# Performance work log

Hardware: AMD Instinct MI355X
Metric: run time of the kernel (lower is better)

Reference implementation:

```python
import jax, jax.numpy as jnp
import numpy as np

N = 50000
E = 800000
IN_DIM = 128
HEADS = 8
OUT_DIM = 32
NEG_SLOPE = 0.2


def setup_inputs() -> dict:
    key = jax.random.key(0)
    k1, k2, k3, k4, k5 = jax.random.split(key, 5)
    x = jax.random.normal(k1, (N, IN_DIM), dtype=jnp.float32)
    edge_index = jax.random.randint(k2, (2, E), 0, N, dtype=jnp.int64)
    batch = jnp.zeros((N,), dtype=jnp.int64)
    # GATConv params: glorot-style scale
    W = jax.random.normal(k3, (IN_DIM, HEADS * OUT_DIM), dtype=jnp.float32) * (1.0 / np.sqrt(IN_DIM))
    att_src = jax.random.normal(k4, (HEADS, OUT_DIM), dtype=jnp.float32) * (1.0 / np.sqrt(OUT_DIM))
    att_dst = jax.random.normal(k5, (HEADS, OUT_DIM), dtype=jnp.float32) * (1.0 / np.sqrt(OUT_DIM))
    bias = jnp.zeros((OUT_DIM,), dtype=jnp.float32)
    return {"x": x, "edge_index": edge_index, "batch": batch,
            "W": W, "att_src": att_src, "att_dst": att_dst, "bias": bias}


def reference(x, edge_index, batch, W, att_src, att_dst, bias):
    n = x.shape[0]
    h = (x @ W).reshape(n, HEADS, OUT_DIM)            # [N, H, C]
    a_src = jnp.einsum('nhc,hc->nh', h, att_src)       # [N, H]
    a_dst = jnp.einsum('nhc,hc->nh', h, att_dst)       # [N, H]
    # add self-loops (PyG default add_self_loops=True)
    loops = jnp.arange(n, dtype=edge_index.dtype)
    src = jnp.concatenate([edge_index[0], loops])
    dst = jnp.concatenate([edge_index[1], loops])
    e = jax.nn.leaky_relu(a_src[src] + a_dst[dst], NEG_SLOPE)  # [E+N, H]
    # scatter-softmax over incoming edges of each dst node
    m = jax.ops.segment_max(e, dst, num_segments=n)    # [N, H]
    m = jax.lax.stop_gradient(m)
    ex = jnp.exp(e - m[dst])
    denom = jax.ops.segment_sum(ex, dst, num_segments=n)
    alpha = ex / denom[dst]                            # [E+N, H]
    msg = h[src] * alpha[..., None]                    # [E+N, H, C]
    out = jax.ops.segment_sum(msg, dst, num_segments=n)  # [N, H, C]
    out = out.mean(axis=1) + bias                      # concat=False -> head mean
    return out
```

## Files before the change

kernel.cpp:

```cpp
#include <hip/hip_runtime.h>

#define IN_DIM 128
#define HC 256
#define HEADS 8
#define OUT_DIM 32
#define NEG_SLOPE 0.2f

typedef unsigned short ushort_t;
typedef unsigned int uint_t;
typedef __attribute__((ext_vector_type(8))) short bf16x8;
typedef __attribute__((ext_vector_type(4))) float floatx4;

__device__ inline ushort_t f2bf(float f) {
    uint_t u = __float_as_uint(f);
    u = (u + 0x7FFF + ((u >> 16) & 1)) >> 16;
    return (ushort_t)u;
}
__device__ inline float bf2f(ushort_t u) {
    return __uint_as_float(((uint_t)u) << 16);
}

__global__ __launch_bounds__(256) void prep_w(const float* __restrict__ W,
                                              ushort_t* __restrict__ Wf,
                                              int* __restrict__ deg, int N) {
    int t = blockIdx.x * 256 + threadIdx.x;
    int lane = t & 63;
    int ks = (t >> 6) & 3;
    int nt = t >> 8;
    int n = nt * 16 + (lane & 15);
    int k0 = ks * 32 + (lane >> 4) * 8;
    ushort_t v[8];
#pragma unroll
    for (int j = 0; j < 8; j++) v[j] = f2bf(W[(size_t)(k0 + j) * HC + n]);
    uint4 pk;
    pk.x = v[0] | ((uint_t)v[1] << 16);
    pk.y = v[2] | ((uint_t)v[3] << 16);
    pk.z = v[4] | ((uint_t)v[5] << 16);
    pk.w = v[6] | ((uint_t)v[7] << 16);
    *(uint4*)&Wf[(size_t)t * 8] = pk;
    for (int i = t; i < N; i += 4096) deg[i] = 0;
}

__global__ __launch_bounds__(256) void gemm_count(const float* __restrict__ x,
                                                  const ushort_t* __restrict__ Wf,
                                                  const float* __restrict__ att_s,
                                                  const float* __restrict__ att_d,
                                                  ushort_t* __restrict__ h2,
                                                  float* __restrict__ a_src,
                                                  float* __restrict__ a_dst,
                                                  const int* __restrict__ edst,
                                                  int* __restrict__ deg,
                                                  ushort_t* __restrict__ rank,
                                                  int N, int E, int gemm_blocks) {
    __shared__ ushort_t xs[128 * 136];
    const int bid = blockIdx.x;
    const int tid = threadIdx.x;

    if (bid >= gemm_blocks) {
        int i = (bid - gemm_blocks) * 256 + tid;
        int base = i * 4;
        if (base + 3 < E) {
            int4 d = *(const int4*)&edst[base];
            rank[base + 0] = (ushort_t)atomicAdd(&deg[d.x], 1);
            rank[base + 1] = (ushort_t)atomicAdd(&deg[d.y], 1);
            rank[base + 2] = (ushort_t)atomicAdd(&deg[d.z], 1);
            rank[base + 3] = (ushort_t)atomicAdd(&deg[d.w], 1);
        } else {
            for (int j = base; j < E; j++) rank[j] = (ushort_t)atomicAdd(&deg[edst[j]], 1);
        }
        return;
    }

    const int row0 = (bid >> 1) * 128;
    const int colhalf = bid & 1;
#pragma unroll
    for (int i = 0; i < 16; i++) {
        int slot = tid + i * 256;
        int r = slot >> 5, kq = slot & 31;
        int gr = row0 + r;
        float4 v = (gr < N) ? *(const float4*)&x[(size_t)gr * IN_DIM + kq * 4]
                            : make_float4(0.f, 0.f, 0.f, 0.f);
        uint2 pk;
        pk.x = f2bf(v.x) | ((uint_t)f2bf(v.y) << 16);
        pk.y = f2bf(v.z) | ((uint_t)f2bf(v.w) << 16);
        *(uint2*)&xs[r * 136 + kq * 4] = pk;
    }
    __syncthreads();

    const int lane = tid & 63;
    const int w = tid >> 6;
    const int wm = (w & 1) * 64;
    const int colblk = colhalf * 128 + (w >> 1) * 64;
    const int m15 = lane & 15, quad = lane >> 4;

    floatx4 acc[4][4] = {};
#pragma unroll
    for (int ks = 0; ks < 4; ks++) {
        bf16x8 a[4], b[4];
#pragma unroll
        for (int mt = 0; mt < 4; mt++)
            a[mt] = *(const bf16x8*)&xs[(wm + mt * 16 + m15) * 136 + ks * 32 + quad * 8];
#pragma unroll
        for (int nt = 0; nt < 4; nt++) {
            int ntg = (colblk >> 4) + nt;
            b[nt] = *(const bf16x8*)&Wf[(size_t)(((ntg * 4 + ks) * 64) + lane) * 8];
        }
#pragma unroll
        for (int mt = 0; mt < 4; mt++)
#pragma unroll
            for (int nt = 0; nt < 4; nt++)
                acc[mt][nt] = __builtin_amdgcn_mfma_f32_16x16x32_bf16(a[mt], b[nt], acc[mt][nt], 0, 0, 0);
    }

    const int cbase = colblk + m15;
    const int head0 = colblk >> 5;
    float as0 = att_s[colblk + m15],      as1 = att_s[colblk + 16 + m15];
    float as2 = att_s[colblk + 32 + m15], as3 = att_s[colblk + 48 + m15];
    float ad0 = att_d[colblk + m15],      ad1 = att_d[colblk + 16 + m15];
    float ad2 = att_d[colblk + 32 + m15], ad3 = att_d[colblk + 48 + m15];
#pragma unroll
    for (int mt = 0; mt < 4; mt++) {
#pragma unroll
        for (int reg = 0; reg < 4; reg++) {
            int gr = row0 + wm + mt * 16 + quad * 4 + reg;
            float sA = acc[mt][0][reg] * as0 + acc[mt][1][reg] * as1;
            float sB = acc[mt][2][reg] * as2 + acc[mt][3][reg] * as3;
            float dA = acc[mt][0][reg] * ad0 + acc[mt][1][reg] * ad1;
            float dB = acc[mt][2][reg] * ad2 + acc[mt][3][reg] * ad3;
#pragma unroll
            for (int off = 1; off < 16; off <<= 1) {
                sA += __shfl_xor(sA, off, 64);
                sB += __shfl_xor(sB, off, 64);
                dA += __shfl_xor(dA, off, 64);
                dB += __shfl_xor(dB, off, 64);
            }
            if (gr < N) {
#pragma unroll
                for (int nt = 0; nt < 4; nt++)
                    h2[(size_t)gr * HC + cbase + nt * 16] = f2bf(acc[mt][nt][reg]);
                if (m15 == 0) {
                    a_src[gr * HEADS + head0] = sA;
                    a_src[gr * HEADS + head0 + 1] = sB;
                    a_dst[gr * HEADS + head0] = dA;
                    a_dst[gr * HEADS + head0 + 1] = dB;
                }
            }
        }
    }
}

__global__ __launch_bounds__(1024) void scan_pass1(const int* __restrict__ deg,
                                                   int* __restrict__ rs,
                                                   int* __restrict__ bsum, int N) {
    __shared__ int wsum[16], wexcl[16];
    int tid = threadIdx.x, lane = tid & 63, w = tid >> 6;
    int base = blockIdx.x * 4096 + tid * 4;
    int v[4];
#pragma unroll
    for (int j = 0; j < 4; j++) v[j] = (base + j < N) ? deg[base + j] : 0;
    int s = v[0] + v[1] + v[2] + v[3];
    int xsc = s;
#pragma unroll
    for (int off = 1; off < 64; off <<= 1) {
        int t = __shfl_up(xsc, off, 64);
        if (lane >= off) xsc += t;
    }
    if (lane == 63) wsum[w] = xsc;
    __syncthreads();
    if (w == 0 && lane < 16) {
        int y = wsum[lane], z = y;
#pragma unroll
        for (int off = 1; off < 16; off <<= 1) {
            int t = __shfl_up(z, off, 64);
            if (lane >= off) z += t;
        }
        wexcl[lane] = z - y;
        if (lane == 15) bsum[blockIdx.x] = z;
    }
    __syncthreads();
    int e = wexcl[w] + (xsc - s);
#pragma unroll
    for (int j = 0; j < 4; j++) {
        if (base + j < N) rs[base + j] = e;
        e += v[j];
    }
}

__global__ __launch_bounds__(256) void scan_pass23(int* __restrict__ rs,
                                                   const int* __restrict__ bsum,
                                                   int N, int nb) {
    __shared__ int soff, stot;
    int tid = threadIdx.x;
    if (tid < 64) {
        int v = (tid < nb) ? bsum[tid] : 0;
        int incl = v;
#pragma unroll
        for (int off = 1; off < 64; off <<= 1) {
            int t = __shfl_up(incl, off, 64);
            if (tid >= off) incl += t;
        }
        int chunk = blockIdx.x >> 4;
        int off_ = __shfl(incl - v, chunk, 64);
        int tot_ = __shfl(incl, nb - 1, 64);
        if (tid == 0) { soff = off_; stot = tot_; }
    }
    __syncthreads();
    int i = blockIdx.x * 256 + tid;
    if (i < N) rs[i] += soff;
    if (i == N) rs[N] = stot;
}

__global__ void scatter_edges(const int* __restrict__ src, const int* __restrict__ dst,
                              const ushort_t* __restrict__ rank,
                              const int* __restrict__ row_start,
                              ushort_t* __restrict__ csr_src, int E) {
    int i = blockIdx.x * 256 + threadIdx.x;
    int base = i * 4;
    if (base + 3 < E) {
        int4 s = *(const int4*)&src[base];
        int4 d = *(const int4*)&dst[base];
        ushort4 r = *(const ushort4*)&rank[base];
        csr_src[row_start[d.x] + r.x] = (ushort_t)s.x;
        csr_src[row_start[d.y] + r.y] = (ushort_t)s.y;
        csr_src[row_start[d.z] + r.z] = (ushort_t)s.z;
        csr_src[row_start[d.w] + r.w] = (ushort_t)s.w;
    } else {
        for (int j = base; j < E; j++)
            csr_src[row_start[dst[j]] + rank[j]] = (ushort_t)src[j];
    }
}

__global__ __launch_bounds__(256) void aggregate(const ushort_t* __restrict__ h2,
                                                 const float* __restrict__ a_src,
                                                 const float* __restrict__ a_dst,
                                                 const int* __restrict__ row_start,
                                                 const ushort_t* __restrict__ csr_src,
                                                 const float* __restrict__ bias,
                                                 float* __restrict__ out, int N) {
    int wave = threadIdx.x >> 6;
    int lane = threadIdx.x & 63;
    int n = blockIdx.x * 4 + wave;
    if (n >= N) return;
    int head = lane >> 3;
    int coff = head * OUT_DIM + (lane & 7) * 4;

    float adst = a_dst[n * HEADS + head];
    float e = a_src[n * HEADS + head] + adst;
    e = fmaxf(e, NEG_SLOPE * e);
    float p = __expf(e);
    ushort4 hv = *(const ushort4*)&h2[(size_t)n * HC + coff];
    float ax = p * bf2f(hv.x), ay = p * bf2f(hv.y), az = p * bf2f(hv.z), aw = p * bf2f(hv.w);
    float l = p;

    int kb = __builtin_amdgcn_readfirstlane(row_start[n]);
    int ke = __builtin_amdgcn_readfirstlane(row_start[n + 1]);
    int k = kb;
    for (; k + 7 < ke; k += 8) {
        int sidx[8];
        ushort4 g[8];
        float ev[8];
#pragma unroll
        for (int j = 0; j < 8; j++)
            sidx[j] = __builtin_amdgcn_readfirstlane((int)csr_src[k + j]);
#pragma unroll
        for (int j = 0; j < 8; j++) {
            g[j] = *(const ushort4*)&h2[(size_t)sidx[j] * HC + coff];
            ev[j] = a_src[sidx[j] * HEADS + head];
        }
#pragma unroll
        for (int j = 0; j < 8; j++) {
            float ej = ev[j] + adst;
            ej = fmaxf(ej, NEG_SLOPE * ej);
            float pj = __expf(ej);
            ax += pj * bf2f(g[j].x);
            ay += pj * bf2f(g[j].y);
            az += pj * bf2f(g[j].z);
            aw += pj * bf2f(g[j].w);
            l += pj;
        }
    }
    for (; k < ke; k++) {
        int s0 = __builtin_amdgcn_readfirstlane((int)csr_src[k]);
        float e0 = a_src[s0 * HEADS + head] + adst;
        ushort4 g0 = *(const ushort4*)&h2[(size_t)s0 * HC + coff];
        e0 = fmaxf(e0, NEG_SLOPE * e0);
        float p0 = __expf(e0);
        ax += p0 * bf2f(g0.x); ay += p0 * bf2f(g0.y);
        az += p0 * bf2f(g0.z); aw += p0 * bf2f(g0.w);
        l += p0;
    }

    float inv = 1.f / l;
    float rx = ax * inv, ry = ay * inv, rz = az * inv, rw = aw * inv;
#pragma unroll
    for (int off = 8; off < 64; off <<= 1) {
        rx += __shfl_xor(rx, off, 64);
        ry += __shfl_xor(ry, off, 64);
        rz += __shfl_xor(rz, off, 64);
        rw += __shfl_xor(rw, off, 64);
    }
    if (head == 0) {
        int c4 = (lane & 7) * 4;
        float4 b = *(const float4*)&bias[c4];
        float4 o = make_float4(0.125f * rx + b.x, 0.125f * ry + b.y,
                               0.125f * rz + b.z, 0.125f * rw + b.w);
        *(float4*)&out[(size_t)n * OUT_DIM + c4] = o;
    }
}

extern "C" void kernel_launch(void* const* d_in, const int* in_sizes, int n_in,
                              void* d_out, int out_size, void* d_ws, size_t ws_size,
                              hipStream_t stream) {
    const float* x       = (const float*)d_in[0];
    const int*   eidx    = (const int*)d_in[1];
    const float* W       = (const float*)d_in[3];
    const float* att_src = (const float*)d_in[4];
    const float* att_dst = (const float*)d_in[5];
    const float* bias    = (const float*)d_in[6];
    float* out = (float*)d_out;

    const int N = in_sizes[0] / IN_DIM;
    const int E = in_sizes[1] / 2;
    const int* esrc = eidx;
    const int* edst = eidx + E;

    char* wsb = (char*)d_ws;
    size_t off = 0;
    auto alloc = [&](size_t bytes) -> void* {
        void* p = wsb + off;
        off = (off + bytes + 255) & ~(size_t)255;
        return p;
    };
    ushort_t* h2       = (ushort_t*)alloc((size_t)N * HC * 2);
    ushort_t* Wf       = (ushort_t*)alloc((size_t)IN_DIM * HC * 2);
    float*    a_src    = (float*)alloc((size_t)N * HEADS * 4);
    float*    a_dst    = (float*)alloc((size_t)N * HEADS * 4);
    int*      deg      = (int*)alloc((size_t)N * 4);
    int*      row_start= (int*)alloc((size_t)(N + 1) * 4);
    ushort_t* rank     = (ushort_t*)alloc((size_t)E * 2);
    ushort_t* csr_src  = (ushort_t*)alloc((size_t)E * 2);
    const int nb = (N + 4095) / 4096;
    int*      bsum     = (int*)alloc((size_t)(nb + 1) * 4);

    const int gemm_blocks = ((N + 127) / 128) * 2;
    const int count_blocks = (E / 4 + 255) / 256;

    hipLaunchKernelGGL(prep_w, dim3(16), dim3(256), 0, stream, W, Wf, deg, N);
    hipLaunchKernelGGL(gemm_count, dim3(gemm_blocks + count_blocks), dim3(256), 0, stream,
                       x, Wf, att_src, att_dst, h2, a_src, a_dst, edst, deg, rank,
                       N, E, gemm_blocks);
    hipLaunchKernelGGL(scan_pass1, dim3(nb), dim3(1024), 0, stream, deg, row_start, bsum, N);
    hipLaunchKernelGGL(scan_pass23, dim3((N + 256) / 256), dim3(256), 0, stream,
                       row_start, bsum, N, nb);
    hipLaunchKernelGGL(scatter_edges, dim3((E / 4 + 255) / 256), dim3(256), 0, stream,
                       esrc, edst, rank, row_start, csr_src, E);
    hipLaunchKernelGGL(aggregate, dim3((N + 3) / 4), dim3(256), 0, stream,
                       h2, a_src, a_dst, row_start, csr_src, bias, out, N);
}
```

Before: 232.2 us.

## Split fused GEMM/count kernel, pad aggregate tail loop, enlarge aggregate blocks

Separates the combined GEMM-plus-degree-count launch back into two kernels, so the GEMM uses a 2D grid and the atomic counting runs as its own launch. The aggregate kernel drops its scalar remainder loop and instead pads the last group of 8 edges with clamped indices and zero weights. It also doubles the block size to 8 waves per block. This gives up the overlap between GEMM and atomics that the fused launch provided, while simplifying the tail handling and cutting the number of aggregate blocks.

Result: slower. 243.6 us (+4.9%).

```diff
diff --git a/kernel.cpp b/kernel.cpp
--- a/kernel.cpp
+++ b/kernel.cpp
@@ -41,38 +41,16 @@
     for (int i = t; i < N; i += 4096) deg[i] = 0;
 }
 
-__global__ __launch_bounds__(256) void gemm_count(const float* __restrict__ x,
-                                                  const ushort_t* __restrict__ Wf,
-                                                  const float* __restrict__ att_s,
-                                                  const float* __restrict__ att_d,
-                                                  ushort_t* __restrict__ h2,
-                                                  float* __restrict__ a_src,
-                                                  float* __restrict__ a_dst,
-                                                  const int* __restrict__ edst,
-                                                  int* __restrict__ deg,
-                                                  ushort_t* __restrict__ rank,
-                                                  int N, int E, int gemm_blocks) {
+__global__ __launch_bounds__(256) void gemm_mfma(const float* __restrict__ x,
+                                                 const ushort_t* __restrict__ Wf,
+                                                 const float* __restrict__ att_s,
+                                                 const float* __restrict__ att_d,
+                                                 ushort_t* __restrict__ h2,
+                                                 float* __restrict__ a_src,
+                                                 float* __restrict__ a_dst, int N) {
     __shared__ ushort_t xs[128 * 136];
-    const int bid = blockIdx.x;
     const int tid = threadIdx.x;
-
-    if (bid >= gemm_blocks) {
-        int i = (bid - gemm_blocks) * 256 + tid;
-        int base = i * 4;
-        if (base + 3 < E) {
-            int4 d = *(const int4*)&edst[base];
-            rank[base + 0] = (ushort_t)atomicAdd(&deg[d.x], 1);
-            rank[base + 1] = (ushort_t)atomicAdd(&deg[d.y], 1);
-            rank[base + 2] = (ushort_t)atomicAdd(&deg[d.z], 1);
-            rank[base + 3] = (ushort_t)atomicAdd(&deg[d.w], 1);
-        } else {
-            for (int j = base; j < E; j++) rank[j] = (ushort_t)atomicAdd(&deg[edst[j]], 1);
-        }
-        return;
-    }
-
-    const int row0 = (bid >> 1) * 128;
-    const int colhalf = bid & 1;
+    const int row0 = blockIdx.x * 128;
 #pragma unroll
     for (int i = 0; i < 16; i++) {
         int slot = tid + i * 256;
@@ -90,7 +68,7 @@
     const int lane = tid & 63;
     const int w = tid >> 6;
     const int wm = (w & 1) * 64;
-    const int colblk = colhalf * 128 + (w >> 1) * 64;
+    const int colblk = blockIdx.y * 128 + (w >> 1) * 64;
     const int m15 = lane & 15, quad = lane >> 4;
 
     floatx4 acc[4][4] = {};
@@ -146,6 +124,21 @@
                 }
             }
         }
+    }
+}
+
+__global__ void count_rank(const int* __restrict__ dst, int* __restrict__ deg,
+                           ushort_t* __restrict__ rank, int E) {
+    int i = blockIdx.x * 256 + threadIdx.x;
+    int base = i * 4;
+    if (base + 3 < E) {
+        int4 d = *(const int4*)&dst[base];
+        rank[base + 0] = (ushort_t)atomicAdd(&deg[d.x], 1);
+        rank[base + 1] = (ushort_t)atomicAdd(&deg[d.y], 1);
+        rank[base + 2] = (ushort_t)atomicAdd(&deg[d.z], 1);
+        rank[base + 3] = (ushort_t)atomicAdd(&deg[d.w], 1);
+    } else {
+        for (int j = base; j < E; j++) rank[j] = (ushort_t)atomicAdd(&deg[dst[j]], 1);
     }
 }
 
@@ -230,7 +223,7 @@
     }
 }
 
-__global__ __launch_bounds__(256) void aggregate(const ushort_t* __restrict__ h2,
+__global__ __launch_bounds__(512) void aggregate(const ushort_t* __restrict__ h2,
                                                  const float* __restrict__ a_src,
                                                  const float* __restrict__ a_dst,
                                                  const int* __restrict__ row_start,
@@ -239,7 +232,7 @@
                                                  float* __restrict__ out, int N) {
     int wave = threadIdx.x >> 6;
     int lane = threadIdx.x & 63;
-    int n = blockIdx.x * 4 + wave;
+    int n = blockIdx.x * 8 + wave;
     if (n >= N) return;
     int head = lane >> 3;
     int coff = head * OUT_DIM + (lane & 7) * 4;
@@ -254,14 +247,16 @@
 
     int kb = __builtin_amdgcn_readfirstlane(row_start[n]);
     int ke = __builtin_amdgcn_readfirstlane(row_start[n + 1]);
-    int k = kb;
-    for (; k + 7 < ke; k += 8) {
+    for (int k = kb; k < ke; k += 8) {
         int sidx[8];
         ushort4 g[8];
         float ev[8];
 #pragma unroll
-        for (int j = 0; j < 8; j++)
-            sidx[j] = __builtin_amdgcn_readfirstlane((int)csr_src[k + j]);
+        for (int j = 0; j < 8; j++) {
+            int kk = k + j;
+            int kc = (kk < ke) ? kk : (ke - 1);
+            sidx[j] = __builtin_amdgcn_readfirstlane((int)csr_src[kc]);
+        }
 #pragma unroll
         for (int j = 0; j < 8; j++) {
             g[j] = *(const ushort4*)&h2[(size_t)sidx[j] * HC + coff];
@@ -271,23 +266,13 @@
         for (int j = 0; j < 8; j++) {
             float ej = ev[j] + adst;
             ej = fmaxf(ej, NEG_SLOPE * ej);
-            float pj = __expf(ej);
+            float pj = (k + j < ke) ? __expf(ej) : 0.f;
             ax += pj * bf2f(g[j].x);
             ay += pj * bf2f(g[j].y);
             az += pj * bf2f(g[j].z);
             aw += pj * bf2f(g[j].w);
             l += pj;
         }
-    }
-    for (; k < ke; k++) {
-        int s0 = __builtin_amdgcn_readfirstlane((int)csr_src[k]);
-        float e0 = a_src[s0 * HEADS + head] + adst;
-        ushort4 g0 = *(const ushort4*)&h2[(size_t)s0 * HC + coff];
-        e0 = fmaxf(e0, NEG_SLOPE * e0);
-        float p0 = __expf(e0);
-        ax += p0 * bf2f(g0.x); ay += p0 * bf2f(g0.y);
-        az += p0 * bf2f(g0.z); aw += p0 * bf2f(g0.w);
-        l += p0;
     }
 
     float inv = 1.f / l;
@@ -342,18 +327,16 @@
     const int nb = (N + 4095) / 4096;
     int*      bsum     = (int*)alloc((size_t)(nb + 1) * 4);
 
-    const int gemm_blocks = ((N + 127) / 128) * 2;
-    const int count_blocks = (E / 4 + 255) / 256;
-
     hipLaunchKernelGGL(prep_w, dim3(16), dim3(256), 0, stream, W, Wf, deg, N);
-    hipLaunchKernelGGL(gemm_count, dim3(gemm_blocks + count_blocks), dim3(256), 0, stream,
-                       x, Wf, att_src, att_dst, h2, a_src, a_dst, edst, deg, rank,
-                       N, E, gemm_blocks);
+    hipLaunchKernelGGL(gemm_mfma, dim3((N + 127) / 128, 2), dim3(256), 0, stream,
+                       x, Wf, att_src, att_dst, h2, a_src, a_dst, N);
+    hipLaunchKernelGGL(count_rank, dim3((E / 4 + 255) / 256), dim3(256), 0, stream,
+                       edst, deg, rank, E);
     hipLaunchKernelGGL(scan_pass1, dim3(nb), dim3(1024), 0, stream, deg, row_start, bsum, N);
     hipLaunchKernelGGL(scan_pass23, dim3((N + 256) / 256), dim3(256), 0, stream,
                        row_start, bsum, N, nb);
     hipLaunchKernelGGL(scatter_edges, dim3((E / 4 + 255) / 256), dim3(256), 0, stream,
                        esrc, edst, rank, row_start, csr_src, E);
-    hipLaunchKernelGGL(aggregate, dim3((N + 3) / 4), dim3(256), 0, stream,
+    hipLaunchKernelGGL(aggregate, dim3((N + 7) / 8), dim3(512), 0, stream,
                        h2, a_src, a_dst, row_start, csr_src, bias, out, N);
 }
```

## Fuse graph build and aggregation into one cooperative kernel with grid syncs

Applied to the files above, without the earlier changes.

Replaces the count, scan, scatter and aggregate kernels with a single cooperative persistent kernel of 1024 blocks that separates phases with grid.sync(). The GEMM is split off into its own launch and no longer overlaps with degree counting. The goal is to cut the launch gaps between the small graph-building kernels. In exchange it adds grid-wide barrier cost, loses the GEMM/count overlap, and the aggregation runs under a fixed grid size with a grid-stride loop.

New measurement: 664.0 us. 2.86x slower.

```diff
diff --git a/kernel.cpp b/kernel.cpp
--- a/kernel.cpp
+++ b/kernel.cpp
@@ -1,10 +1,14 @@
 #include <hip/hip_runtime.h>
+#include <hip/hip_cooperative_groups.h>
+
+namespace cg = cooperative_groups;
 
 #define IN_DIM 128
 #define HC 256
 #define HEADS 8
 #define OUT_DIM 32
 #define NEG_SLOPE 0.2f
+#define GRID_B 1024
 
 typedef unsigned short ushort_t;
 typedef unsigned int uint_t;
@@ -41,38 +45,16 @@
     for (int i = t; i < N; i += 4096) deg[i] = 0;
 }
 
-__global__ __launch_bounds__(256) void gemm_count(const float* __restrict__ x,
-                                                  const ushort_t* __restrict__ Wf,
-                                                  const float* __restrict__ att_s,
-                                                  const float* __restrict__ att_d,
-                                                  ushort_t* __restrict__ h2,
-                                                  float* __restrict__ a_src,
-                                                  float* __restrict__ a_dst,
-                                                  const int* __restrict__ edst,
-                                                  int* __restrict__ deg,
-                                                  ushort_t* __restrict__ rank,
-                                                  int N, int E, int gemm_blocks) {
+__global__ __launch_bounds__(256) void gemm_mfma(const float* __restrict__ x,
+                                                 const ushort_t* __restrict__ Wf,
+                                                 const float* __restrict__ att_s,
+                                                 const float* __restrict__ att_d,
+                                                 ushort_t* __restrict__ h2,
+                                                 float* __restrict__ a_src,
+                                                 float* __restrict__ a_dst, int N) {
     __shared__ ushort_t xs[128 * 136];
-    const int bid = blockIdx.x;
     const int tid = threadIdx.x;
-
-    if (bid >= gemm_blocks) {
-        int i = (bid - gemm_blocks) * 256 + tid;
-        int base = i * 4;
-        if (base + 3 < E) {
-            int4 d = *(const int4*)&edst[base];
-            rank[base + 0] = (ushort_t)atomicAdd(&deg[d.x], 1);
-            rank[base + 1] = (ushort_t)atomicAdd(&deg[d.y], 1);
-            rank[base + 2] = (ushort_t)atomicAdd(&deg[d.z], 1);
-            rank[base + 3] = (ushort_t)atomicAdd(&deg[d.w], 1);
-        } else {
-            for (int j = base; j < E; j++) rank[j] = (ushort_t)atomicAdd(&deg[edst[j]], 1);
-        }
-        return;
-    }
-
-    const int row0 = (bid >> 1) * 128;
-    const int colhalf = bid & 1;
+    const int row0 = blockIdx.x * 128;
 #pragma unroll
     for (int i = 0; i < 16; i++) {
         int slot = tid + i * 256;
@@ -90,7 +72,7 @@
     const int lane = tid & 63;
     const int w = tid >> 6;
     const int wm = (w & 1) * 64;
-    const int colblk = colhalf * 128 + (w >> 1) * 64;
+    const int colblk = blockIdx.y * 128 + (w >> 1) * 64;
     const int m15 = lane & 15, quad = lane >> 4;
 
     floatx4 acc[4][4] = {};
@@ -149,162 +131,180 @@
     }
 }
 
-__global__ __launch_bounds__(1024) void scan_pass1(const int* __restrict__ deg,
-                                                   int* __restrict__ rs,
-                                                   int* __restrict__ bsum, int N) {
-    __shared__ int wsum[16], wexcl[16];
-    int tid = threadIdx.x, lane = tid & 63, w = tid >> 6;
-    int base = blockIdx.x * 4096 + tid * 4;
-    int v[4];
-#pragma unroll
-    for (int j = 0; j < 4; j++) v[j] = (base + j < N) ? deg[base + j] : 0;
-    int s = v[0] + v[1] + v[2] + v[3];
-    int xsc = s;
-#pragma unroll
-    for (int off = 1; off < 64; off <<= 1) {
-        int t = __shfl_up(xsc, off, 64);
-        if (lane >= off) xsc += t;
-    }
-    if (lane == 63) wsum[w] = xsc;
-    __syncthreads();
-    if (w == 0 && lane < 16) {
-        int y = wsum[lane], z = y;
-#pragma unroll
-        for (int off = 1; off < 16; off <<= 1) {
-            int t = __shfl_up(z, off, 64);
-            if (lane >= off) z += t;
-        }
-        wexcl[lane] = z - y;
-        if (lane == 15) bsum[blockIdx.x] = z;
-    }
-    __syncthreads();
-    int e = wexcl[w] + (xsc - s);
-#pragma unroll
-    for (int j = 0; j < 4; j++) {
-        if (base + j < N) rs[base + j] = e;
-        e += v[j];
-    }
-}
-
-__global__ __launch_bounds__(256) void scan_pass23(int* __restrict__ rs,
-                                                   const int* __restrict__ bsum,
-                                                   int N, int nb) {
-    __shared__ int soff, stot;
-    int tid = threadIdx.x;
+__global__ __launch_bounds__(256) void fused_graph(const int* __restrict__ esrc,
+                                                   const int* __restrict__ edst,
+                                                   int* __restrict__ deg,
+                                                   ushort_t* __restrict__ rank,
+                                                   int* __restrict__ row_start,
+                                                   int* __restrict__ bsum,
+                                                   ushort_t* __restrict__ csr_src,
+                                                   const ushort_t* __restrict__ h2,
+                                                   const float* __restrict__ a_src,
+                                                   const float* __restrict__ a_dst,
+                                                   const float* __restrict__ bias,
+                                                   float* __restrict__ out,
+                                                   int N, int E) {
+    cg::grid_group grid = cg::this_grid();
+    const int tid = threadIdx.x;
+    const int bid = blockIdx.x;
+    const int idx = bid * 256 + tid;
+    const int tcount = GRID_B * 256;
+    const int lane = tid & 63, w = tid >> 6;
+    const int QC = (E + 3) >> 2;
+    const int nc = (N + 1023) >> 10;
+
+    for (int i = idx; i < QC; i += tcount) {
+        int base = i * 4;
+        if (base + 3 < E) {
+            int4 d = *(const int4*)&edst[base];
+            rank[base + 0] = (ushort_t)atomicAdd(&deg[d.x], 1);
+            rank[base + 1] = (ushort_t)atomicAdd(&deg[d.y], 1);
+            rank[base + 2] = (ushort_t)atomicAdd(&deg[d.z], 1);
+            rank[base + 3] = (ushort_t)atomicAdd(&deg[d.w], 1);
+        } else {
+            for (int j = base; j < E; j++) rank[j] = (ushort_t)atomicAdd(&deg[edst[j]], 1);
+        }
+    }
+    grid.sync();
+
+    __shared__ int wsum[4], wexcl2[4];
+    if (bid < nc) {
+        int base = bid * 1024 + tid * 4;
+        int v[4];
+#pragma unroll
+        for (int j = 0; j < 4; j++) v[j] = (base + j < N) ? deg[base + j] : 0;
+        int s = v[0] + v[1] + v[2] + v[3];
+        int xsc = s;
+#pragma unroll
+        for (int off = 1; off < 64; off <<= 1) {
+            int t = __shfl_up(xsc, off, 64);
+            if (lane >= off) xsc += t;
+        }
+        if (lane == 63) wsum[w] = xsc;
+        __syncthreads();
+        if (w == 0 && lane < 4) {
+            int y = wsum[lane], z = y;
+#pragma unroll
+            for (int off = 1; off < 4; off <<= 1) {
+                int t = __shfl_up(z, off, 64);
+                if (lane >= off) z += t;
+            }
+            wexcl2[lane] = z - y;
+            if (lane == 3) bsum[bid] = z;
+        }
+        __syncthreads();
+        int e = wexcl2[w] + (xsc - s);
+#pragma unroll
+        for (int j = 0; j < 4; j++) {
+            if (base + j < N) row_start[base + j] = e;
+            e += v[j];
+        }
+    }
+    grid.sync();
+
+    __shared__ int excl_lds[64];
+    __shared__ int stot;
     if (tid < 64) {
-        int v = (tid < nb) ? bsum[tid] : 0;
-        int incl = v;
+        int vv = (tid < nc) ? bsum[tid] : 0;
+        int incl = vv;
 #pragma unroll
         for (int off = 1; off < 64; off <<= 1) {
             int t = __shfl_up(incl, off, 64);
             if (tid >= off) incl += t;
         }
-        int chunk = blockIdx.x >> 4;
-        int off_ = __shfl(incl - v, chunk, 64);
-        int tot_ = __shfl(incl, nb - 1, 64);
-        if (tid == 0) { soff = off_; stot = tot_; }
+        excl_lds[tid] = incl - vv;
+        if (tid == nc - 1) stot = incl;
     }
     __syncthreads();
-    int i = blockIdx.x * 256 + tid;
-    if (i < N) rs[i] += soff;
-    if (i == N) rs[N] = stot;
-}
-
-__global__ void scatter_edges(const int* __restrict__ src, const int* __restrict__ dst,
-                              const ushort_t* __restrict__ rank,
-                              const int* __restrict__ row_start,
-                              ushort_t* __restrict__ csr_src, int E) {
-    int i = blockIdx.x * 256 + threadIdx.x;
-    int base = i * 4;
-    if (base + 3 < E) {
-        int4 s = *(const int4*)&src[base];
-        int4 d = *(const int4*)&dst[base];
-        ushort4 r = *(const ushort4*)&rank[base];
-        csr_src[row_start[d.x] + r.x] = (ushort_t)s.x;
-        csr_src[row_start[d.y] + r.y] = (ushort_t)s.y;
-        csr_src[row_start[d.z] + r.z] = (ushort_t)s.z;
-        csr_src[row_start[d.w] + r.w] = (ushort_t)s.w;
-    } else {
-        for (int j = base; j < E; j++)
-            csr_src[row_start[dst[j]] + rank[j]] = (ushort_t)src[j];
-    }
-}
-
-__global__ __launch_bounds__(256) void aggregate(const ushort_t* __restrict__ h2,
-                                                 const float* __restrict__ a_src,
-                                                 const float* __restrict__ a_dst,
-                                                 const int* __restrict__ row_start,
-                                                 const ushort_t* __restrict__ csr_src,
-                                                 const float* __restrict__ bias,
-                                                 float* __restrict__ out, int N) {
-    int wave = threadIdx.x >> 6;
-    int lane = threadIdx.x & 63;
-    int n = blockIdx.x * 4 + wave;
-    if (n >= N) return;
-    int head = lane >> 3;
-    int coff = head * OUT_DIM + (lane & 7) * 4;
-
-    float adst = a_dst[n * HEADS + head];
-    float e = a_src[n * HEADS + head] + adst;
-    e = fmaxf(e, NEG_SLOPE * e);
-    float p = __expf(e);
-    ushort4 hv = *(const ushort4*)&h2[(size_t)n * HC + coff];
-    float ax = p * bf2f(hv.x), ay = p * bf2f(hv.y), az = p * bf2f(hv.z), aw = p * bf2f(hv.w);
-    float l = p;
-
-    int kb = __builtin_amdgcn_readfirstlane(row_start[n]);
-    int ke = __builtin_amdgcn_readfirstlane(row_start[n + 1]);
-    int k = kb;
-    for (; k + 7 < ke; k += 8) {
-        int sidx[8];
-        ushort4 g[8];
-        float ev[8];
-#pragma unroll
-        for (int j = 0; j < 8; j++)
-            sidx[j] = __builtin_amdgcn_readfirstlane((int)csr_src[k + j]);
-#pragma unroll
-        for (int j = 0; j < 8; j++) {
-            g[j] = *(const ushort4*)&h2[(size_t)sidx[j] * HC + coff];
-            ev[j] = a_src[sidx[j] * HEADS + head];
-        }
-#pragma unroll
-        for (int j = 0; j < 8; j++) {
-            float ej = ev[j] + adst;
-            ej = fmaxf(ej, NEG_SLOPE * ej);
-            float pj = __expf(ej);
-            ax += pj * bf2f(g[j].x);
-            ay += pj * bf2f(g[j].y);
-            az += pj * bf2f(g[j].z);
-            aw += pj * bf2f(g[j].w);
-            l += pj;
-        }
-    }
-    for (; k < ke; k++) {
-        int s0 = __builtin_amdgcn_readfirstlane((int)csr_src[k]);
-        float e0 = a_src[s0 * HEADS + head] + adst;
-        ushort4 g0 = *(const ushort4*)&h2[(size_t)s0 * HC + coff];
-        e0 = fmaxf(e0, NEG_SLOPE * e0);
-        float p0 = __expf(e0);
-        ax += p0 * bf2f(g0.x); ay += p0 * bf2f(g0.y);
-        az += p0 * bf2f(g0.z); aw += p0 * bf2f(g0.w);
-        l += p0;
-    }
-
-    float inv = 1.f / l;
-    float rx = ax * inv, ry = ay * inv, rz = az * inv, rw = aw * inv;
-#pragma unroll
-    for (int off = 8; off < 64; off <<= 1) {
-        rx += __shfl_xor(rx, off, 64);
-        ry += __shfl_xor(ry, off, 64);
-        rz += __shfl_xor(rz, off, 64);
-        rw += __shfl_xor(rw, off, 64);
-    }
-    if (head == 0) {
-        int c4 = (lane & 7) * 4;
-        float4 b = *(const float4*)&bias[c4];
-        float4 o = make_float4(0.125f * rx + b.x, 0.125f * ry + b.y,
-                               0.125f * rz + b.z, 0.125f * rw + b.w);
-        *(float4*)&out[(size_t)n * OUT_DIM + c4] = o;
+    for (int i = idx; i < N; i += tcount) row_start[i] += excl_lds[i >> 10];
+    if (idx == 0) row_start[N] = stot;
+    grid.sync();
+
+    for (int i = idx; i < QC; i += tcount) {
+        int base = i * 4;
+        if (base + 3 < E) {
+            int4 s4 = *(const int4*)&esrc[base];
+            int4 d4 = *(const int4*)&edst[base];
+            ushort4 r4 = *(const ushort4*)&rank[base];
+            csr_src[row_start[d4.x] + r4.x] = (ushort_t)s4.x;
+            csr_src[row_start[d4.y] + r4.y] = (ushort_t)s4.y;
+            csr_src[row_start[d4.z] + r4.z] = (ushort_t)s4.z;
+            csr_src[row_start[d4.w] + r4.w] = (ushort_t)s4.w;
+        } else {
+            for (int j = base; j < E; j++)
+                csr_src[row_start[edst[j]] + rank[j]] = (ushort_t)esrc[j];
+        }
+    }
+    grid.sync();
+
+    const int head = lane >> 3;
+    const int coff = head * OUT_DIM + (lane & 7) * 4;
+    for (int n0 = bid * 4; n0 < N; n0 += GRID_B * 4) {
+        int n = n0 + w;
+        if (n >= N) continue;
+
+        float adst = a_dst[n * HEADS + head];
+        float e = a_src[n * HEADS + head] + adst;
+        e = fmaxf(e, NEG_SLOPE * e);
+        float p = __expf(e);
+        ushort4 hv = *(const ushort4*)&h2[(size_t)n * HC + coff];
+        float ax = p * bf2f(hv.x), ay = p * bf2f(hv.y), az = p * bf2f(hv.z), aw = p * bf2f(hv.w);
+        float l = p;
+
+        int kb = __builtin_amdgcn_readfirstlane(row_start[n]);
+        int ke = __builtin_amdgcn_readfirstlane(row_start[n + 1]);
+        int k = kb;
+        for (; k + 7 < ke; k += 8) {
+            int sidx[8];
+            ushort4 g[8];
+            float ev[8];
+#pragma unroll
+            for (int j = 0; j < 8; j++)
+                sidx[j] = __builtin_amdgcn_readfirstlane((int)csr_src[k + j]);
+#pragma unroll
+            for (int j = 0; j < 8; j++) {
+                g[j] = *(const ushort4*)&h2[(size_t)sidx[j] * HC + coff];
+                ev[j] = a_src[sidx[j] * HEADS + head];
+            }
+#pragma unroll
+            for (int j = 0; j < 8; j++) {
+                float ej = ev[j] + adst;
+                ej = fmaxf(ej, NEG_SLOPE * ej);
+                float pj = __expf(ej);
+                ax += pj * bf2f(g[j].x);
+                ay += pj * bf2f(g[j].y);
+                az += pj * bf2f(g[j].z);
+                aw += pj * bf2f(g[j].w);
+                l += pj;
+            }
+        }
+        for (; k < ke; k++) {
+            int s0 = __builtin_amdgcn_readfirstlane((int)csr_src[k]);
+            float e0 = a_src[s0 * HEADS + head] + adst;
+            ushort4 g0 = *(const ushort4*)&h2[(size_t)s0 * HC + coff];
+            e0 = fmaxf(e0, NEG_SLOPE * e0);
+            float p0 = __expf(e0);
+            ax += p0 * bf2f(g0.x); ay += p0 * bf2f(g0.y);
+            az += p0 * bf2f(g0.z); aw += p0 * bf2f(g0.w);
+            l += p0;
+        }
+
+        float inv = 1.f / l;
+        float rx = ax * inv, ry = ay * inv, rz = az * inv, rw = aw * inv;
+#pragma unroll
+        for (int off = 8; off < 64; off <<= 1) {
+            rx += __shfl_xor(rx, off, 64);
+            ry += __shfl_xor(ry, off, 64);
+            rz += __shfl_xor(rz, off, 64);
+            rw += __shfl_xor(rw, off, 64);
+        }
+        if (head == 0) {
+            int c4 = (lane & 7) * 4;
+            float4 b = *(const float4*)&bias[c4];
+            float4 o = make_float4(0.125f * rx + b.x, 0.125f * ry + b.y,
+                                   0.125f * rz + b.z, 0.125f * rw + b.w);
+            *(float4*)&out[(size_t)n * OUT_DIM + c4] = o;
+        }
     }
 }
 
@@ -339,21 +339,20 @@
     int*      row_start= (int*)alloc((size_t)(N + 1) * 4);
     ushort_t* rank     = (ushort_t*)alloc((size_t)E * 2);
     ushort_t* csr_src  = (ushort_t*)alloc((size_t)E * 2);
-    const int nb = (N + 4095) / 4096;
-    int*      bsum     = (int*)alloc((size_t)(nb + 1) * 4);
-
-    const int gemm_blocks = ((N + 127) / 128) * 2;
-    const int count_blocks = (E / 4 + 255) / 256;
+    const int nc = (N + 1023) / 1024;
+    int*      bsum     = (int*)alloc((size_t)(nc + 1) * 4);
 
     hipLaunchKernelGGL(prep_w, dim3(16), dim3(256), 0, stream, W, Wf, deg, N);
-    hipLaunchKernelGGL(gemm_count, dim3(gemm_blocks + count_blocks), dim3(256), 0, stream,
-                       x, Wf, att_src, att_dst, h2, a_src, a_dst, edst, deg, rank,
-                       N, E, gemm_blocks);
-    hipLaunchKernelGGL(scan_pass1, dim3(nb), dim3(1024), 0, stream, deg, row_start, bsum, N);
-    hipLaunchKernelGGL(scan_pass23, dim3((N + 256) / 256), dim3(256), 0, stream,
-                       row_start, bsum, N, nb);
-    hipLaunchKernelGGL(scatter_edges, dim3((E / 4 + 255) / 256), dim3(256), 0, stream,
-                       esrc, edst, rank, row_start, csr_src, E);
-    hipLaunchKernelGGL(aggregate, dim3((N + 3) / 4), dim3(256), 0, stream,
-                       h2, a_src, a_dst, row_start, csr_src, bias, out, N);
-}
+    hipLaunchKernelGGL(gemm_mfma, dim3((N + 127) / 128, 2), dim3(256), 0, stream,
+                       x, Wf, att_src, att_dst, h2, a_src, a_dst, N);
+
+    int Nv = N, Ev = E;
+    void* kargs[] = {
+        (void*)&esrc, (void*)&edst, (void*)&deg, (void*)&rank,
+        (void*)&row_start, (void*)&bsum, (void*)&csr_src,
+        (void*)&h2, (void*)&a_src, (void*)&a_dst, (void*)&bias,
+        (void*)&out, (void*)&Nv, (void*)&Ev
+    };
+    hipLaunchCooperativeKernel(reinterpret_cast<void*>(fused_graph),
+                               dim3(GRID_B), dim3(256), kargs, 0, stream);
+}
```
